# Kernel optimization log

Hardware: AMD Instinct MI355X
Metric: run time of the kernel (lower is better)

Reference implementation:

```python
import jax, jax.numpy as jnp
import numpy as np


def setup_inputs() -> dict:
    key = jax.random.key(0)
    ks = jax.random.split(key, 10)
    B, C, T, H, W = 8, 128, 8, 32, 32
    Cq = C // 8
    return {
        "x": jax.random.normal(ks[0], (B, C, T, H, W), dtype=jnp.float32),
        "Wq": jax.random.normal(ks[1], (Cq, C), dtype=jnp.float32) * (1.0 / np.sqrt(C)),
        "bq": jax.random.normal(ks[2], (Cq,), dtype=jnp.float32) * 0.02,
        "Wk": jax.random.normal(ks[3], (Cq, C), dtype=jnp.float32) * (1.0 / np.sqrt(C)),
        "bk": jax.random.normal(ks[4], (Cq,), dtype=jnp.float32) * 0.02,
        "Wv": jax.random.normal(ks[5], (C, C), dtype=jnp.float32) * (1.0 / np.sqrt(C)),
        "bv": jax.random.normal(ks[6], (C,), dtype=jnp.float32) * 0.02,
        "gamma_pam": jax.random.normal(ks[7], (1,), dtype=jnp.float32),
        "gamma_cam": jax.random.normal(ks[8], (1,), dtype=jnp.float32),
        "gamma_tim": jax.random.normal(ks[9], (1,), dtype=jnp.float32),
    }


def reference(x, Wq, bq, Wk, bk, Wv, bv, gamma_pam, gamma_cam, gamma_tim):
    B, C, T, H, W = x.shape
    HW = H * W

    # ---- PAM: position attention over HW, feature dim = (C//8)*T ----
    # 1x1x1 Conv3d == per-position channel matmul
    q = jnp.einsum('bcthw,oc->bothw', x, Wq) + bq[None, :, None, None, None]
    k = jnp.einsum('bcthw,oc->bothw', x, Wk) + bk[None, :, None, None, None]
    v = jnp.einsum('bcthw,oc->bothw', x, Wv) + bv[None, :, None, None, None]
    qf = q.reshape(B, -1, HW)   # [B, (C//8)*T, HW]
    kf = k.reshape(B, -1, HW)
    vf = v.reshape(B, -1, HW)   # [B, C*T, HW]
    energy = jnp.einsum('bcn,bcm->bnm', qf, kf)          # [B, HW, HW]
    attn = jax.nn.softmax(energy, axis=-1)
    # out = bmm(v, attn^T)
    pam = jnp.einsum('bcm,bnm->bcn', vf, attn).reshape(B, C, T, H, W)
    pam = gamma_pam * pam + x

    # ---- CAM: channel attention (C x C) with negated-energy softmax ----
    xc = x.reshape(B, C, -1)                              # [B, C, T*HW]
    e = jnp.einsum('bcn,bdn->bcd', xc, xc)                # [B, C, C]
    e = jnp.max(e, axis=-1, keepdims=True) - e
    a = jax.nn.softmax(e, axis=-1)
    cam = jnp.einsum('bcd,bdn->bcn', a, xc).reshape(B, C, T, H, W)
    cam = gamma_cam * cam + x

    # ---- TIM: temporal attention (T x T) with negated-energy softmax ----
    xt = jnp.transpose(x, (0, 2, 1, 3, 4)).reshape(B, T, -1)  # [B, T, C*HW]
    e = jnp.einsum('btn,bsn->bts', xt, xt)                # [B, T, T]
    e = jnp.max(e, axis=-1, keepdims=True) - e
    a = jax.nn.softmax(e, axis=-1)
    tim = jnp.einsum('bts,bsn->btn', a, xt).reshape(B, T, C, H, W)
    tim = jnp.transpose(tim, (0, 2, 1, 3, 4))
    tim = gamma_tim * tim + x

    return pam + cam + tim
```

## Files before the change

### kernel.cpp

```cpp
#include <hip/hip_runtime.h>
#include <cstdint>

typedef unsigned short u16;
typedef __attribute__((ext_vector_type(8))) short bf16x8;
typedef __attribute__((ext_vector_type(4))) float f32x4;

constexpr int B_  = 8;
constexpr int C_  = 128;
constexpr int T_  = 8;
constexpr int HW_ = 1024;
constexpr int P_  = T_ * HW_;
constexpr int F_  = 128;
constexpr int CT_ = C_ * T_;

static __device__ __forceinline__ u16 f2bf(float f) {
    union { float f; unsigned u; } v; v.f = f;
    unsigned r = v.u + 0x7fffu + ((v.u >> 16) & 1u);
    return (u16)(r >> 16);
}
static __device__ __forceinline__ float bf2f(u16 h) {
    union { unsigned u; float f; } v; v.u = ((unsigned)h) << 16;
    return v.f;
}

#define GLOAD16(src, dst)                                                     \
    __builtin_amdgcn_global_load_lds(                                         \
        (const __attribute__((address_space(1))) void*)(src),                 \
        (__attribute__((address_space(3))) void*)(dst), 16, 0, 0)

__global__ __launch_bounds__(256)
void k_prep(const float* __restrict__ x, u16* __restrict__ xT,
            u16* __restrict__ xhi, u16* __restrict__ xlo,
            const float* __restrict__ Wq, const float* __restrict__ bq,
            const float* __restrict__ Wk, const float* __restrict__ bk,
            const float* __restrict__ Wv, const float* __restrict__ bv,
            u16* __restrict__ Wall, float* __restrict__ ball)
{
    const int tid = threadIdx.x;
    if (blockIdx.x == 64) {
        if (blockIdx.y != 0) return;
        for (int i = tid; i < 20480; i += 256) {
            int oc = i >> 7, c = i & 127;
            float w;
            if (oc < 16)      w = Wq[oc * 128 + c];
            else if (oc < 32) w = Wk[(oc - 16) * 128 + c];
            else              w = Wv[(oc - 32) * 128 + c];
            Wall[i] = f2bf(w);
        }
        if (tid < 160) {
            float bb;
            if (tid < 16)      bb = bq[tid];
            else if (tid < 32) bb = bk[tid - 16];
            else               bb = bv[tid - 32];
            ball[tid] = bb;
        }
        return;
    }

    __shared__ char sy[32768];
    const int b  = blockIdx.y;
    const int p0 = blockIdx.x * 128;

    #pragma unroll
    for (int r = 0; r < 16; r++) {
        int lin = r * 256 + tid;
        int c = lin >> 5, j4 = (lin & 31) << 2;
        size_t gi = ((size_t)(b * C_ + c)) * P_ + p0 + j4;
        float4 xv = *(const float4*)&x[gi];
        float a4[4] = {xv.x, xv.y, xv.z, xv.w};
        ushort4 h, l;
        h.x = f2bf(a4[0]); h.y = f2bf(a4[1]);
        h.z = f2bf(a4[2]); h.w = f2bf(a4[3]);
        l.x = f2bf(a4[0] - bf2f(h.x)); l.y = f2bf(a4[1] - bf2f(h.y));
        l.z = f2bf(a4[2] - bf2f(h.z)); l.w = f2bf(a4[3] - bf2f(h.w));
        *(ushort4*)&xhi[gi] = h;
        *(ushort4*)&xlo[gi] = l;
        #pragma unroll
        for (int u = 0; u < 4; u++) {
            int pi = j4 + u;
            int byte = pi * 256 + ((c * 2) ^ (((pi >> 2) & 15) << 4));
            *(u16*)(sy + byte) = (u == 0) ? h.x : (u == 1) ? h.y
                               : (u == 2) ? h.z : h.w;
        }
    }
    __syncthreads();
    #pragma unroll
    for (int r = 0; r < 8; r++) {
        int lin = r * 256 + tid;
        int pi = lin >> 4, ci8 = (lin & 15) << 3;
        bf16x8 v = *(const bf16x8*)(sy + pi * 256 +
                                    ((ci8 * 2) ^ (((pi >> 2) & 15) << 4)));
        *(bf16x8*)&xT[((size_t)(b * P_ + p0 + pi)) * C_ + ci8] = v;
    }
}

__global__ __launch_bounds__(256)
void k_qkv(const u16* __restrict__ xT, const u16* __restrict__ Wall,
           const float* __restrict__ ball,
           u16* __restrict__ qt, u16* __restrict__ kt, u16* __restrict__ v16)
{
    __shared__ char Ws[40960];
    const int b  = blockIdx.y;
    const int p0 = blockIdx.x * 128;
    const int tid = threadIdx.x, lane = tid & 63, w = tid >> 6;

    #pragma unroll
    for (int i = 0; i < 10; i++) {
        int ch  = w * 10 + i;
        int row = ch * 4 + (lane >> 4);
        int col = ((lane & 15) ^ (row & 7)) * 8;
        GLOAD16(Wall + row * 128 + col, Ws + ch * 1024);
    }

    const u16* Bb = xT + ((size_t)(b * P_ + p0 + w * 32)) * F_;
    bf16x8 bg[4][2];
    #pragma unroll
    for (int ks = 0; ks < 4; ks++)
        #pragma unroll
        for (int ni = 0; ni < 2; ni++)
            bg[ks][ni] = *(const bf16x8*)(Bb +
                (size_t)(ni * 16 + (lane & 15)) * F_ + ks * 32 + (lane >> 4) * 8);
    __syncthreads();

    f32x4 acc[10][2];
    #pragma unroll
    for (int mi = 0; mi < 10; mi++) {
        acc[mi][0] = (f32x4){0.f, 0.f, 0.f, 0.f};
        acc[mi][1] = (f32x4){0.f, 0.f, 0.f, 0.f};
    }

    #pragma unroll
    for (int mi = 0; mi < 10; mi++) {
        #pragma unroll
        for (int ks = 0; ks < 4; ks++) {
            int row  = mi * 16 + (lane & 15);
            int slot = (ks * 4 + (lane >> 4)) ^ (row & 7);
            bf16x8 af = *(const bf16x8*)(Ws + row * 256 + slot * 16);
            acc[mi][0] = __builtin_amdgcn_mfma_f32_16x16x32_bf16(
                af, bg[ks][0], acc[mi][0], 0, 0, 0);
            acc[mi][1] = __builtin_amdgcn_mfma_f32_16x16x32_bf16(
                af, bg[ks][1], acc[mi][1], 0, 0, 0);
        }
    }

    const int t      = p0 >> 10;
    const int hwbase = (p0 & 1023) + w * 32;
    #pragma unroll
    for (int mi = 0; mi < 10; mi++)
        #pragma unroll
        for (int ni = 0; ni < 2; ni++)
            #pragma unroll
            for (int r = 0; r < 4; r++) {
                int oc = mi * 16 + (lane >> 4) * 4 + r;
                int hw = hwbase + ni * 16 + (lane & 15);
                u16 bv16 = f2bf(acc[mi][ni][r] + ball[oc]);
                if (mi == 0)
                    qt[((size_t)b * HW_ + hw) * F_ + oc * 8 + t] = bv16;
                else if (mi == 1)
                    kt[((size_t)b * HW_ + hw) * F_ + (oc - 16) * 8 + t] = bv16;
                else
                    v16[((size_t)(b * C_ + oc - 32)) * P_ + t * HW_ + hw] = bv16;
            }
}

__global__ __launch_bounds__(256)
void k_energy(const u16* __restrict__ qt, const u16* __restrict__ kt,
              float* __restrict__ E)
{
    __shared__ char As[32768];
    __shared__ char Bs[32768];
    const int b  = blockIdx.z;
    const int n0 = blockIdx.y * 128, m0 = blockIdx.x * 128;
    const int tid = threadIdx.x, lane = tid & 63, w = tid >> 6;
    const u16* qb = qt + (size_t)b * HW_ * F_;
    const u16* kb = kt + (size_t)b * HW_ * F_;

    #pragma unroll
    for (int i = 0; i < 8; i++) {
        int c    = w * 8 + i;
        int row  = c * 4 + (lane >> 4);
        int col  = ((lane & 15) ^ (row & 7)) * 8;
        GLOAD16(qb + (size_t)(n0 + row) * F_ + col, As + c * 1024);
        GLOAD16(kb + (size_t)(m0 + row) * F_ + col, Bs + c * 1024);
    }
    __syncthreads();

    const int wr = w >> 1, wc = w & 1;
    f32x4 acc[4][4];
    #pragma unroll
    for (int mi = 0; mi < 4; mi++)
        #pragma unroll
        for (int ni = 0; ni < 4; ni++) acc[mi][ni] = (f32x4){0.f, 0.f, 0.f, 0.f};

    #pragma unroll
    for (int ks = 0; ks < 4; ks++) {
        bf16x8 af[4], bg[4];
        #pragma unroll
        for (int mi = 0; mi < 4; mi++) {
            int row  = wr * 64 + mi * 16 + (lane & 15);
            int slot = (ks * 4 + (lane >> 4)) ^ (row & 7);
            af[mi] = *(const bf16x8*)(As + row * 256 + slot * 16);
            int rb  = wc * 64 + mi * 16 + (lane & 15);
            int sb  = (ks * 4 + (lane >> 4)) ^ (rb & 7);
            bg[mi] = *(const bf16x8*)(Bs + rb * 256 + sb * 16);
        }
        #pragma unroll
        for (int mi = 0; mi < 4; mi++)
            #pragma unroll
            for (int ni = 0; ni < 4; ni++)
                acc[mi][ni] = __builtin_amdgcn_mfma_f32_16x16x32_bf16(
                    af[mi], bg[ni], acc[mi][ni], 0, 0, 0);
    }

    float* Eb = E + (size_t)b * HW_ * HW_;
    #pragma unroll
    for (int mi = 0; mi < 4; mi++)
        #pragma unroll
        for (int ni = 0; ni < 4; ni++)
            #pragma unroll
            for (int r = 0; r < 4; r++)
                Eb[(size_t)(n0 + wr * 64 + mi * 16 + (lane >> 4) * 4 + r) * HW_
                   + m0 + wc * 64 + ni * 16 + (lane & 15)] = acc[mi][ni][r];
}

__global__ __launch_bounds__(256)
void k_softmax(const float* __restrict__ E, u16* __restrict__ A16)
{
    const float* e = E + (size_t)blockIdx.x * HW_;
    const int tid = threadIdx.x;
    float4 v = ((const float4*)e)[tid];
    float m = fmaxf(fmaxf(v.x, v.y), fmaxf(v.z, v.w));
    #pragma unroll
    for (int off = 32; off; off >>= 1) m = fmaxf(m, __shfl_xor(m, off));
    __shared__ float s1[4], s2[4];
    if ((tid & 63) == 0) s1[tid >> 6] = m;
    __syncthreads();
    m = fmaxf(fmaxf(s1[0], s1[1]), fmaxf(s1[2], s1[3]));
    v.x = __expf(v.x - m); v.y = __expf(v.y - m);
    v.z = __expf(v.z - m); v.w = __expf(v.w - m);
    float s = v.x + v.y + v.z + v.w;
    #pragma unroll
    for (int off = 32; off; off >>= 1) s += __shfl_xor(s, off);
    if ((tid & 63) == 0) s2[tid >> 6] = s;
    __syncthreads();
    s = s2[0] + s2[1] + s2[2] + s2[3];
    float inv = 1.0f / s;
    ushort4 pk;
    pk.x = f2bf(v.x * inv); pk.y = f2bf(v.y * inv);
    pk.z = f2bf(v.z * inv); pk.w = f2bf(v.w * inv);
    ((ushort4*)(A16 + (size_t)blockIdx.x * HW_))[tid] = pk;
}

__global__ __launch_bounds__(256)
void k_pv(const u16* __restrict__ v16, const u16* __restrict__ A16,
          const float* __restrict__ gamma_pam, u16* __restrict__ pam16)
{
    __shared__ char As[2][16384];
    __shared__ char Bs[2][16384];
    const int b   = blockIdx.z;
    const int ct0 = blockIdx.y * 128, n0 = blockIdx.x * 128;
    const int tid = threadIdx.x, lane = tid & 63, w = tid >> 6;
    const u16* vb = v16 + (size_t)b * CT_ * HW_;
    const u16* ab = A16 + (size_t)b * HW_ * HW_;

    const int s_row = (lane >> 3);
    const int s_col = ((lane & 7) ^ ((lane >> 3) & 7)) * 8;

    const int wr = w >> 1, wc = w & 1;
    f32x4 acc[4][4];
    #pragma unroll
    for (int mi = 0; mi < 4; mi++)
        #pragma unroll
        for (int ni = 0; ni < 4; ni++) acc[mi][ni] = (f32x4){0.f, 0.f, 0.f, 0.f};

    #pragma unroll
    for (int i = 0; i < 4; i++) {
        int c = w * 4 + i;
        int row = c * 8 + s_row;
        GLOAD16(vb + (size_t)(ct0 + row) * HW_ + s_col, As[0] + c * 1024);
        GLOAD16(ab + (size_t)(n0  + row) * HW_ + s_col, Bs[0] + c * 1024);
    }
    __syncthreads();

    int cur = 0;
    for (int it = 0; it < 16; ++it) {
        if (it < 15) {
            int mc = (it + 1) * 64;
            #pragma unroll
            for (int i = 0; i < 4; i++) {
                int c = w * 4 + i;
                int row = c * 8 + s_row;
                GLOAD16(vb + (size_t)(ct0 + row) * HW_ + mc + s_col,
                        As[cur ^ 1] + c * 1024);
                GLOAD16(ab + (size_t)(n0  + row) * HW_ + mc + s_col,
                        Bs[cur ^ 1] + c * 1024);
            }
        }
        const char* Ac = As[cur];
        const char* Bc = Bs[cur];
        #pragma unroll
        for (int ks = 0; ks < 2; ks++) {
            bf16x8 af[4], bg[4];
            #pragma unroll
            for (int mi = 0; mi < 4; mi++) {
                int row  = wr * 64 + mi * 16 + (lane & 15);
                int slot = (ks * 4 + (lane >> 4)) ^ (row & 7);
                af[mi] = *(const bf16x8*)(Ac + row * 128 + slot * 16);
                int rb  = wc * 64 + mi * 16 + (lane & 15);
                int sb  = (ks * 4 + (lane >> 4)) ^ (rb & 7);
                bg[mi] = *(const bf16x8*)(Bc + rb * 128 + sb * 16);
            }
            #pragma unroll
            for (int mi = 0; mi < 4; mi++)
                #pragma unroll
                for (int ni = 0; ni < 4; ni++)
                    acc[mi][ni] = __builtin_amdgcn_mfma_f32_16x16x32_bf16(
                        af[mi], bg[ni], acc[mi][ni], 0, 0, 0);
        }
        __syncthreads();
        cur ^= 1;
    }

    const float gp = gamma_pam[0];
    u16* ob = pam16 + (size_t)b * CT_ * HW_;
    #pragma unroll
    for (int mi = 0; mi < 4; mi++)
        #pragma unroll
        for (int ni = 0; ni < 4; ni++)
            #pragma unroll
            for (int r = 0; r < 4; r++)
                ob[(size_t)(ct0 + wr * 64 + mi * 16 + (lane >> 4) * 4 + r) * HW_
                   + n0 + wc * 64 + ni * 16 + (lane & 15)] =
                    f2bf(gp * acc[mi][ni][r]);
}

__global__ __launch_bounds__(256)
void k_cam_gram(const u16* __restrict__ xhi, const u16* __restrict__ xlo,
                float* __restrict__ part)
{
    __shared__ char Sh[32768];
    __shared__ char Sl[32768];
    const int b = blockIdx.y, ch = blockIdx.x;
    const int tid = threadIdx.x, lane = tid & 63, w = tid >> 6;
    const u16* hb = xhi + (size_t)b * C_ * P_;
    const u16* lb = xlo + (size_t)b * C_ * P_;

    f32x4 acc[8][2];
    #pragma unroll
    for (int mi = 0; mi < 8; mi++) {
        acc[mi][0] = (f32x4){0.f, 0.f, 0.f, 0.f};
        acc[mi][1] = (f32x4){0.f, 0.f, 0.f, 0.f};
    }

    for (int kc = 0; kc < 2; kc++) {
        int n0 = ch * 256 + kc * 128;
        #pragma unroll
        for (int i = 0; i < 8; i++) {
            int c4  = w * 8 + i;
            int row = c4 * 4 + (lane >> 4);
            int col = ((lane & 15) ^ (row & 7)) * 8;
            GLOAD16(hb + (size_t)row * P_ + n0 + col, Sh + c4 * 1024);
            GLOAD16(lb + (size_t)row * P_ + n0 + col, Sl + c4 * 1024);
        }
        __syncthreads();
        #pragma unroll
        for (int ks = 0; ks < 4; ks++) {
            bf16x8 bh[2], bl[2];
            #pragma unroll
            for (int ni = 0; ni < 2; ni++) {
                int rb = w * 32 + ni * 16 + (lane & 15);
                int sb = (ks * 4 + (lane >> 4)) ^ (rb & 7);
                bh[ni] = *(const bf16x8*)(Sh + rb * 256 + sb * 16);
                bl[ni] = *(const bf16x8*)(Sl + rb * 256 + sb * 16);
            }
            #pragma unroll
            for (int mi = 0; mi < 8; mi++) {
                int ra = mi * 16 + (lane & 15);
                int sa = (ks * 4 + (lane >> 4)) ^ (ra & 7);
                bf16x8 ah = *(const bf16x8*)(Sh + ra * 256 + sa * 16);
                bf16x8 al = *(const bf16x8*)(Sl + ra * 256 + sa * 16);
                #pragma unroll
                for (int ni = 0; ni < 2; ni++) {
                    acc[mi][ni] = __builtin_amdgcn_mfma_f32_16x16x32_bf16(
                        ah, bh[ni], acc[mi][ni], 0, 0, 0);
                    acc[mi][ni] = __builtin_amdgcn_mfma_f32_16x16x32_bf16(
                        ah, bl[ni], acc[mi][ni], 0, 0, 0);
                    acc[mi][ni] = __builtin_amdgcn_mfma_f32_16x16x32_bf16(
                        al, bh[ni], acc[mi][ni], 0, 0, 0);
                }
            }
        }
        __syncthreads();
    }

    float* pb = part + ((size_t)(b * 32 + ch)) * 16384;
    #pragma unroll
    for (int mi = 0; mi < 8; mi++)
        #pragma unroll
        for (int ni = 0; ni < 2; ni++)
            #pragma unroll
            for (int r = 0; r < 4; r++) {
                int c = mi * 16 + (lane >> 4) * 4 + r;
                int d = w * 32 + ni * 16 + (lane & 15);
                pb[c * 128 + d] = acc[mi][ni][r];
            }
}

__global__ __launch_bounds__(128)
void k_cam_reduce(const float* __restrict__ part,
                  const float* __restrict__ gamma_cam, u16* __restrict__ acam16)
{
    const int b = blockIdx.y, c = blockIdx.x;
    const int d = threadIdx.x;
    float s = 0.f;
    for (int ch = 0; ch < 32; ch++)
        s += part[(((size_t)(b * 32 + ch)) * C_ + c) * C_ + d];
    float mn = s;
    #pragma unroll
    for (int off = 32; off; off >>= 1) mn = fminf(mn, __shfl_xor(mn, off));
    __shared__ float m1[2], m2[2];
    if ((d & 63) == 0) m1[d >> 6] = mn;
    __syncthreads();
    mn = fminf(m1[0], m1[1]);
    float p = __expf(mn - s);
    float sum = p;
    #pragma unroll
    for (int off = 32; off; off >>= 1) sum += __shfl_xor(sum, off);
    if ((d & 63) == 0) m2[d >> 6] = sum;
    __syncthreads();
    sum = m2[0] + m2[1];
    acam16[((size_t)(b * C_ + c)) * C_ + d] = f2bf(gamma_cam[0] * p / sum);
}

__global__ __launch_bounds__(256)
void k_tim_gram(const float* __restrict__ x, float* __restrict__ e_t)
{
    const int b = blockIdx.y, c = blockIdx.x;
    const int tid = threadIdx.x;
    const float* xb = x + ((size_t)(b * C_ + c)) * P_;
    float acc[8][8] = {};
    for (int r = 0; r < 4; r++) {
        int hw = r * 256 + tid;
        float xv[8];
        #pragma unroll
        for (int t = 0; t < 8; t++) xv[t] = xb[t * HW_ + hw];
        #pragma unroll
        for (int t = 0; t < 8; t++)
            #pragma unroll
            for (int s2 = 0; s2 < 8; s2++)
                acc[t][s2] += xv[t] * xv[s2];
    }
    __shared__ float sm[4][64];
    const int lane = tid & 63, wid = tid >> 6;
    #pragma unroll
    for (int u = 0; u < 64; u++) {
        float vv = acc[u >> 3][u & 7];
        #pragma unroll
        for (int off = 32; off; off >>= 1) vv += __shfl_xor(vv, off);
        if (lane == 0) sm[wid][u] = vv;
    }
    __syncthreads();
    if (tid < 64) {
        float vv = sm[0][tid] + sm[1][tid] + sm[2][tid] + sm[3][tid];
        atomicAdd(&e_t[b * 64 + tid], vv);
    }
}

__global__ __launch_bounds__(256)
void k_xprime(const float* __restrict__ x, const float* __restrict__ e_t,
              const float* __restrict__ gamma_tim, u16* __restrict__ Xp)
{
    const int b = blockIdx.y, c = blockIdx.x;
    const size_t base = ((size_t)(b * C_ + c)) * P_;
    const int tid = threadIdx.x;
    const float gt = gamma_tim[0];

    float4 xv[8];
    #pragma unroll
    for (int t = 0; t < 8; t++)
        xv[t] = *(const float4*)&x[base + t * HW_ + tid * 4];

    #pragma unroll
    for (int t = 0; t < 8; t++) {
        float e[8];
        #pragma unroll
        for (int s = 0; s < 8; s++) e[s] = e_t[b * 64 + t * 8 + s];
        float mn = e[0];
        #pragma unroll
        for (int s = 1; s < 8; s++) mn = fminf(mn, e[s]);
        float p[8], sum = 0.f;
        #pragma unroll
        for (int s = 0; s < 8; s++) { p[s] = __expf(mn - e[s]); sum += p[s]; }
        float inv = gt / sum;

        float4 o = make_float4(3.f * xv[t].x, 3.f * xv[t].y,
                               3.f * xv[t].z, 3.f * xv[t].w);
        #pragma unroll
        for (int s = 0; s < 8; s++) {
            float wgt = p[s] * inv;
            o.x += wgt * xv[s].x; o.y += wgt * xv[s].y;
            o.z += wgt * xv[s].z; o.w += wgt * xv[s].w;
        }
        ushort4 pk;
        pk.x = f2bf(o.x); pk.y = f2bf(o.y); pk.z = f2bf(o.z); pk.w = f2bf(o.w);
        *(ushort4*)&Xp[base + t * HW_ + tid * 4] = pk;
    }
}

__global__ __launch_bounds__(256)
void k_cam_av(const u16* __restrict__ acam16, const u16* __restrict__ xT,
              const u16* __restrict__ Xp, const u16* __restrict__ pam16,
              float* __restrict__ out)
{
    const int b  = blockIdx.y;
    const int p0 = blockIdx.x * 128;
    const int tid = threadIdx.x, lane = tid & 63, w = tid >> 6;

    const u16* Ab = acam16 + (size_t)b * C_ * C_;
    const u16* Bb = xT + ((size_t)(b * P_ + p0 + w * 32)) * C_;

    f32x4 acc[8][2];
    #pragma unroll
    for (int mi = 0; mi < 8; mi++) {
        acc[mi][0] = (f32x4){0.f, 0.f, 0.f, 0.f};
        acc[mi][1] = (f32x4){0.f, 0.f, 0.f, 0.f};
    }

    bf16x8 bg[4][2];
    #pragma unroll
    for (int ks = 0; ks < 4; ks++)
        #pragma unroll
        for (int ni = 0; ni < 2; ni++)
            bg[ks][ni] = *(const bf16x8*)(Bb +
                (size_t)(ni * 16 + (lane & 15)) * C_ + ks * 32 + (lane >> 4) * 8);

    #pragma unroll
    for (int mi = 0; mi < 8; mi++) {
        #pragma unroll
        for (int ks = 0; ks < 4; ks++) {
            bf16x8 af = *(const bf16x8*)(Ab +
                (size_t)(mi * 16 + (lane & 15)) * C_ + ks * 32 + (lane >> 4) * 8);
            acc[mi][0] = __builtin_amdgcn_mfma_f32_16x16x32_bf16(
                af, bg[ks][0], acc[mi][0], 0, 0, 0);
            acc[mi][1] = __builtin_amdgcn_mfma_f32_16x16x32_bf16(
                af, bg[ks][1], acc[mi][1], 0, 0, 0);
        }
    }

    const int tt = p0 >> 10;
    float* ob = out + (size_t)b * C_ * P_;
    const u16* xp = Xp + (size_t)b * C_ * P_;
    const u16* pb = pam16 + (size_t)b * CT_ * HW_;
    #pragma unroll
    for (int mi = 0; mi < 8; mi++)
        #pragma unroll
        for (int ni = 0; ni < 2; ni++)
            #pragma unroll
            for (int r = 0; r < 4; r++) {
                int c = mi * 16 + (lane >> 4) * 4 + r;
                int p = p0 + w * 32 + ni * 16 + (lane & 15);
                int hw = p & 1023;
                size_t i = (size_t)c * P_ + p;
                float pam = bf2f(pb[((size_t)(c * 8 + tt)) * HW_ + hw]);
                ob[i] = pam + acc[mi][ni][r] + bf2f(xp[i]);
            }
}

extern "C" void kernel_launch(void* const* d_in, const int* in_sizes, int n_in,
                              void* d_out, int out_size, void* d_ws, size_t ws_size,
                              hipStream_t stream)
{
    (void)in_sizes; (void)n_in; (void)out_size; (void)ws_size;
    const float* x  = (const float*)d_in[0];
    const float* Wq = (const float*)d_in[1];
    const float* bq = (const float*)d_in[2];
    const float* Wk = (const float*)d_in[3];
    const float* bk = (const float*)d_in[4];
    const float* Wv = (const float*)d_in[5];
    const float* bv = (const float*)d_in[6];
    const float* gp = (const float*)d_in[7];
    const float* gc = (const float*)d_in[8];
    const float* gt = (const float*)d_in[9];
    float* out = (float*)d_out;
    char*  ws  = (char*)d_ws;

    const size_t MiB = 1u << 20;
    u16*   xT     = (u16*)(ws + 0);
    u16*   v16    = (u16*)(ws + 16 * MiB);
    u16*   xhi    = (u16*)(ws + 32 * MiB);
    u16*   xlo    = (u16*)(ws + 48 * MiB);
    float* Ebuf   = (float*)(ws + 64 * MiB);
    float* part   = (float*)(ws + 64 * MiB);
    u16*   pam16  = (u16*)(ws + 80 * MiB);
    u16*   A16    = (u16*)(ws + 96 * MiB);
    u16*   Xp16   = (u16*)(ws + 96 * MiB);
    u16*   qtb    = (u16*)(ws + 112 * MiB);
    u16*   ktb    = (u16*)(ws + 114 * MiB);
    u16*   acam16 = (u16*)(ws + 116 * MiB);
    u16*   Wall   = (u16*)(ws + 116 * MiB + 65536);
    float* ball   = (float*)(ws + 116 * MiB + 131072);
    float* etim   = (float*)(ws + 116 * MiB + 139264);

    hipMemsetAsync(etim, 0, 512 * sizeof(float), stream);

    k_prep      <<<dim3(65, 8),   256, 0, stream>>>(x, xT, xhi, xlo,
                                                    Wq, bq, Wk, bk, Wv, bv,
                                                    Wall, ball);
    k_qkv       <<<dim3(64, 8),   256, 0, stream>>>(xT, Wall, ball,
                                                    qtb, ktb, v16);
    k_energy    <<<dim3(8, 8, 8), 256, 0, stream>>>(qtb, ktb, Ebuf);
    k_softmax   <<<dim3(8192),    256, 0, stream>>>(Ebuf, A16);
    k_tim_gram  <<<dim3(128, 8),  256, 0, stream>>>(x, etim);
    k_pv        <<<dim3(8, 8, 8), 256, 0, stream>>>(v16, A16, gp, pam16);
    k_xprime    <<<dim3(128, 8),  256, 0, stream>>>(x, etim, gt, Xp16);
    k_cam_gram  <<<dim3(32, 8),   256, 0, stream>>>(xhi, xlo, part);
    k_cam_reduce<<<dim3(128, 8),  128, 0, stream>>>(part, gc, acam16);
    k_cam_av    <<<dim3(64, 8),   256, 0, stream>>>(acam16, xT, Xp16,
                                                    pam16, out);
}
```

Baseline: 266.1 us.

## Fuse energy GEMM with softmax, fold QKV projection into prep, merge weight packing

The PAM energy GEMM and row softmax now run in one kernel, k_attn, which writes only the bf16 attention matrix. This removes the 32 MiB fp32 energy round trip through memory and one launch. The QKV projection moves into k_prep and reads the transposed x tile straight from shared memory, dropping the k_qkv launch and its xT reread. Weight packing moves into k_tim_gram, and biases are read directly instead of being staged. In exchange, k_attn uses only 512 blocks of 16 rows each, reads K from global memory without LDS staging, and k_prep now reads the weights from global memory per wave.

```diff
diff --git a/kernel.cpp b/kernel.cpp
--- a/kernel.cpp
+++ b/kernel.cpp
@@ -29,37 +29,65 @@
         (__attribute__((address_space(3))) void*)(dst), 16, 0, 0)
 
 __global__ __launch_bounds__(256)
+void k_tim_gram(const float* __restrict__ x, float* __restrict__ e_t,
+                const float* __restrict__ Wq, const float* __restrict__ Wk,
+                const float* __restrict__ Wv, u16* __restrict__ Wall)
+{
+    const int b = blockIdx.y, c = blockIdx.x;
+    const int tid = threadIdx.x;
+
+    if (blockIdx.x == 0 && blockIdx.y == 0) {
+        for (int i = tid; i < 20480; i += 256) {
+            int oc = i >> 7, cc = i & 127;
+            float wv;
+            if (oc < 16)      wv = Wq[oc * 128 + cc];
+            else if (oc < 32) wv = Wk[(oc - 16) * 128 + cc];
+            else              wv = Wv[(oc - 32) * 128 + cc];
+            Wall[i] = f2bf(wv);
+        }
+    }
+
+    const float* xb = x + ((size_t)(b * C_ + c)) * P_;
+    float acc[8][8] = {};
+    for (int r = 0; r < 4; r++) {
+        int hw = r * 256 + tid;
+        float xv[8];
+        #pragma unroll
+        for (int t = 0; t < 8; t++) xv[t] = xb[t * HW_ + hw];
+        #pragma unroll
+        for (int t = 0; t < 8; t++)
+            #pragma unroll
+            for (int s2 = 0; s2 < 8; s2++)
+                acc[t][s2] += xv[t] * xv[s2];
+    }
+    __shared__ float sm[4][64];
+    const int lane = tid & 63, wid = tid >> 6;
+    #pragma unroll
+    for (int u = 0; u < 64; u++) {
+        float vv = acc[u >> 3][u & 7];
+        #pragma unroll
+        for (int off = 32; off; off >>= 1) vv += __shfl_xor(vv, off);
+        if (lane == 0) sm[wid][u] = vv;
+    }
+    __syncthreads();
+    if (tid < 64) {
+        float vv = sm[0][tid] + sm[1][tid] + sm[2][tid] + sm[3][tid];
+        atomicAdd(&e_t[b * 64 + tid], vv);
+    }
+}
+
+__global__ __launch_bounds__(256)
 void k_prep(const float* __restrict__ x, u16* __restrict__ xT,
             u16* __restrict__ xhi, u16* __restrict__ xlo,
-            const float* __restrict__ Wq, const float* __restrict__ bq,
-            const float* __restrict__ Wk, const float* __restrict__ bk,
-            const float* __restrict__ Wv, const float* __restrict__ bv,
-            u16* __restrict__ Wall, float* __restrict__ ball)
-{
-    const int tid = threadIdx.x;
-    if (blockIdx.x == 64) {
-        if (blockIdx.y != 0) return;
-        for (int i = tid; i < 20480; i += 256) {
-            int oc = i >> 7, c = i & 127;
-            float w;
-            if (oc < 16)      w = Wq[oc * 128 + c];
-            else if (oc < 32) w = Wk[(oc - 16) * 128 + c];
-            else              w = Wv[(oc - 32) * 128 + c];
-            Wall[i] = f2bf(w);
-        }
-        if (tid < 160) {
-            float bb;
-            if (tid < 16)      bb = bq[tid];
-            else if (tid < 32) bb = bk[tid - 16];
-            else               bb = bv[tid - 32];
-            ball[tid] = bb;
-        }
-        return;
-    }
-
+            const u16* __restrict__ Wall,
+            const float* __restrict__ bq, const float* __restrict__ bk,
+            const float* __restrict__ bv,
+            u16* __restrict__ qt, u16* __restrict__ kt, u16* __restrict__ v16)
+{
     __shared__ char sy[32768];
     const int b  = blockIdx.y;
     const int p0 = blockIdx.x * 128;
+    const int tid = threadIdx.x, lane = tid & 63, w = tid >> 6;
 
     #pragma unroll
     for (int r = 0; r < 16; r++) {
@@ -84,6 +112,7 @@
         }
     }
     __syncthreads();
+
     #pragma unroll
     for (int r = 0; r < 8; r++) {
         int lin = r * 256 + tid;
@@ -92,35 +121,17 @@
                                     ((ci8 * 2) ^ (((pi >> 2) & 15) << 4)));
         *(bf16x8*)&xT[((size_t)(b * P_ + p0 + pi)) * C_ + ci8] = v;
     }
-}
-
-__global__ __launch_bounds__(256)
-void k_qkv(const u16* __restrict__ xT, const u16* __restrict__ Wall,
-           const float* __restrict__ ball,
-           u16* __restrict__ qt, u16* __restrict__ kt, u16* __restrict__ v16)
-{
-    __shared__ char Ws[40960];
-    const int b  = blockIdx.y;
-    const int p0 = blockIdx.x * 128;
-    const int tid = threadIdx.x, lane = tid & 63, w = tid >> 6;
-
-    #pragma unroll
-    for (int i = 0; i < 10; i++) {
-        int ch  = w * 10 + i;
-        int row = ch * 4 + (lane >> 4);
-        int col = ((lane & 15) ^ (row & 7)) * 8;
-        GLOAD16(Wall + row * 128 + col, Ws + ch * 1024);
-    }
-
-    const u16* Bb = xT + ((size_t)(b * P_ + p0 + w * 32)) * F_;
+
     bf16x8 bg[4][2];
     #pragma unroll
     for (int ks = 0; ks < 4; ks++)
         #pragma unroll
-        for (int ni = 0; ni < 2; ni++)
-            bg[ks][ni] = *(const bf16x8*)(Bb +
-                (size_t)(ni * 16 + (lane & 15)) * F_ + ks * 32 + (lane >> 4) * 8);
-    __syncthreads();
+        for (int ni = 0; ni < 2; ni++) {
+            int p  = w * 32 + ni * 16 + (lane & 15);
+            int cb = (ks * 32 + (lane >> 4) * 8) * 2;
+            bg[ks][ni] = *(const bf16x8*)(sy + p * 256 +
+                              (cb ^ (((p >> 2) & 15) << 4)));
+        }
 
     f32x4 acc[10][2];
     #pragma unroll
@@ -133,9 +144,8 @@
     for (int mi = 0; mi < 10; mi++) {
         #pragma unroll
         for (int ks = 0; ks < 4; ks++) {
-            int row  = mi * 16 + (lane & 15);
-            int slot = (ks * 4 + (lane >> 4)) ^ (row & 7);
-            bf16x8 af = *(const bf16x8*)(Ws + row * 256 + slot * 16);
+            bf16x8 af = *(const bf16x8*)(Wall + (mi * 16 + (lane & 15)) * 128
+                                          + ks * 32 + (lane >> 4) * 8);
             acc[mi][0] = __builtin_amdgcn_mfma_f32_16x16x32_bf16(
                 af, bg[ks][0], acc[mi][0], 0, 0, 0);
             acc[mi][1] = __builtin_amdgcn_mfma_f32_16x16x32_bf16(
@@ -153,7 +163,11 @@
             for (int r = 0; r < 4; r++) {
                 int oc = mi * 16 + (lane >> 4) * 4 + r;
                 int hw = hwbase + ni * 16 + (lane & 15);
-                u16 bv16 = f2bf(acc[mi][ni][r] + ball[oc]);
+                float bias;
+                if (mi == 0)      bias = bq[oc];
+                else if (mi == 1) bias = bk[oc - 16];
+                else              bias = bv[oc - 32];
+                u16 bv16 = f2bf(acc[mi][ni][r] + bias);
                 if (mi == 0)
                     qt[((size_t)b * HW_ + hw) * F_ + oc * 8 + t] = bv16;
                 else if (mi == 1)
@@ -164,91 +178,89 @@
 }
 
 __global__ __launch_bounds__(256)
-void k_energy(const u16* __restrict__ qt, const u16* __restrict__ kt,
-              float* __restrict__ E)
-{
-    __shared__ char As[32768];
-    __shared__ char Bs[32768];
-    const int b  = blockIdx.z;
-    const int n0 = blockIdx.y * 128, m0 = blockIdx.x * 128;
+void k_attn(const u16* __restrict__ qt, const u16* __restrict__ kt,
+            u16* __restrict__ A16)
+{
+    const int b  = blockIdx.y;
+    const int n0 = blockIdx.x * 16;
     const int tid = threadIdx.x, lane = tid & 63, w = tid >> 6;
     const u16* qb = qt + (size_t)b * HW_ * F_;
     const u16* kb = kt + (size_t)b * HW_ * F_;
 
-    #pragma unroll
-    for (int i = 0; i < 8; i++) {
-        int c    = w * 8 + i;
-        int row  = c * 4 + (lane >> 4);
-        int col  = ((lane & 15) ^ (row & 7)) * 8;
-        GLOAD16(qb + (size_t)(n0 + row) * F_ + col, As + c * 1024);
-        GLOAD16(kb + (size_t)(m0 + row) * F_ + col, Bs + c * 1024);
-    }
-    __syncthreads();
-
-    const int wr = w >> 1, wc = w & 1;
-    f32x4 acc[4][4];
-    #pragma unroll
-    for (int mi = 0; mi < 4; mi++)
-        #pragma unroll
-        for (int ni = 0; ni < 4; ni++) acc[mi][ni] = (f32x4){0.f, 0.f, 0.f, 0.f};
-
-    #pragma unroll
-    for (int ks = 0; ks < 4; ks++) {
-        bf16x8 af[4], bg[4];
-        #pragma unroll
-        for (int mi = 0; mi < 4; mi++) {
-            int row  = wr * 64 + mi * 16 + (lane & 15);
-            int slot = (ks * 4 + (lane >> 4)) ^ (row & 7);
-            af[mi] = *(const bf16x8*)(As + row * 256 + slot * 16);
-            int rb  = wc * 64 + mi * 16 + (lane & 15);
-            int sb  = (ks * 4 + (lane >> 4)) ^ (rb & 7);
-            bg[mi] = *(const bf16x8*)(Bs + rb * 256 + sb * 16);
-        }
-        #pragma unroll
-        for (int mi = 0; mi < 4; mi++)
-            #pragma unroll
-            for (int ni = 0; ni < 4; ni++)
-                acc[mi][ni] = __builtin_amdgcn_mfma_f32_16x16x32_bf16(
-                    af[mi], bg[ni], acc[mi][ni], 0, 0, 0);
-    }
-
-    float* Eb = E + (size_t)b * HW_ * HW_;
-    #pragma unroll
-    for (int mi = 0; mi < 4; mi++)
-        #pragma unroll
-        for (int ni = 0; ni < 4; ni++)
-            #pragma unroll
-            for (int r = 0; r < 4; r++)
-                Eb[(size_t)(n0 + wr * 64 + mi * 16 + (lane >> 4) * 4 + r) * HW_
-                   + m0 + wc * 64 + ni * 16 + (lane & 15)] = acc[mi][ni][r];
-}
-
-__global__ __launch_bounds__(256)
-void k_softmax(const float* __restrict__ E, u16* __restrict__ A16)
-{
-    const float* e = E + (size_t)blockIdx.x * HW_;
-    const int tid = threadIdx.x;
-    float4 v = ((const float4*)e)[tid];
-    float m = fmaxf(fmaxf(v.x, v.y), fmaxf(v.z, v.w));
-    #pragma unroll
-    for (int off = 32; off; off >>= 1) m = fmaxf(m, __shfl_xor(m, off));
-    __shared__ float s1[4], s2[4];
-    if ((tid & 63) == 0) s1[tid >> 6] = m;
-    __syncthreads();
-    m = fmaxf(fmaxf(s1[0], s1[1]), fmaxf(s1[2], s1[3]));
-    v.x = __expf(v.x - m); v.y = __expf(v.y - m);
-    v.z = __expf(v.z - m); v.w = __expf(v.w - m);
-    float s = v.x + v.y + v.z + v.w;
-    #pragma unroll
-    for (int off = 32; off; off >>= 1) s += __shfl_xor(s, off);
-    if ((tid & 63) == 0) s2[tid >> 6] = s;
-    __syncthreads();
-    s = s2[0] + s2[1] + s2[2] + s2[3];
-    float inv = 1.0f / s;
-    ushort4 pk;
-    pk.x = f2bf(v.x * inv); pk.y = f2bf(v.y * inv);
-    pk.z = f2bf(v.z * inv); pk.w = f2bf(v.w * inv);
-    ((ushort4*)(A16 + (size_t)blockIdx.x * HW_))[tid] = pk;
+    bf16x8 af[4];
+    #pragma unroll
+    for (int ks = 0; ks < 4; ks++)
+        af[ks] = *(const bf16x8*)(qb + (size_t)(n0 + (lane & 15)) * F_
+                                  + ks * 32 + (lane >> 4) * 8);
+
+    f32x4 acc[16];
+    #pragma unroll
+    for (int j = 0; j < 16; j++) acc[j] = (f32x4){0.f, 0.f, 0.f, 0.f};
+
+    #pragma unroll
+    for (int j = 0; j < 16; j++) {
+        const int m0 = w * 256 + j * 16;
+        #pragma unroll
+        for (int ks = 0; ks < 4; ks++) {
+            bf16x8 bg = *(const bf16x8*)(kb + (size_t)(m0 + (lane & 15)) * F_
+                                         + ks * 32 + (lane >> 4) * 8);
+            acc[j] = __builtin_amdgcn_mfma_f32_16x16x32_bf16(
+                af[ks], bg, acc[j], 0, 0, 0);
+        }
+    }
+
+    __shared__ float red[4][16];
+    float rmax[4];
+    #pragma unroll
+    for (int r = 0; r < 4; r++) {
+        float m = acc[0][r];
+        #pragma unroll
+        for (int j = 1; j < 16; j++) m = fmaxf(m, acc[j][r]);
+        #pragma unroll
+        for (int off = 1; off < 16; off <<= 1) m = fmaxf(m, __shfl_xor(m, off));
+        rmax[r] = m;
+    }
+    if ((lane & 15) == 0)
+        #pragma unroll
+        for (int r = 0; r < 4; r++) red[w][(lane >> 4) * 4 + r] = rmax[r];
+    __syncthreads();
+    #pragma unroll
+    for (int r = 0; r < 4; r++) {
+        int row = (lane >> 4) * 4 + r;
+        rmax[r] = fmaxf(fmaxf(red[0][row], red[1][row]),
+                        fmaxf(red[2][row], red[3][row]));
+    }
+    __syncthreads();
+
+    float rsum[4];
+    #pragma unroll
+    for (int r = 0; r < 4; r++) {
+        float s = 0.f;
+        #pragma unroll
+        for (int j = 0; j < 16; j++) {
+            acc[j][r] = __expf(acc[j][r] - rmax[r]);
+            s += acc[j][r];
+        }
+        #pragma unroll
+        for (int off = 1; off < 16; off <<= 1) s += __shfl_xor(s, off);
+        rsum[r] = s;
+    }
+    if ((lane & 15) == 0)
+        #pragma unroll
+        for (int r = 0; r < 4; r++) red[w][(lane >> 4) * 4 + r] = rsum[r];
+    __syncthreads();
+
+    u16* ob = A16 + ((size_t)b * HW_ + n0) * HW_;
+    #pragma unroll
+    for (int r = 0; r < 4; r++) {
+        int row = (lane >> 4) * 4 + r;
+        float inv = 1.0f / (red[0][row] + red[1][row] +
+                            red[2][row] + red[3][row]);
+        #pragma unroll
+        for (int j = 0; j < 16; j++)
+            ob[(size_t)row * HW_ + w * 256 + j * 16 + (lane & 15)] =
+                f2bf(acc[j][r] * inv);
+    }
 }
 
 __global__ __launch_bounds__(256)
@@ -433,40 +445,6 @@
 }
 
 __global__ __launch_bounds__(256)
-void k_tim_gram(const float* __restrict__ x, float* __restrict__ e_t)
-{
-    const int b = blockIdx.y, c = blockIdx.x;
-    const int tid = threadIdx.x;
-    const float* xb = x + ((size_t)(b * C_ + c)) * P_;
-    float acc[8][8] = {};
-    for (int r = 0; r < 4; r++) {
-        int hw = r * 256 + tid;
-        float xv[8];
-        #pragma unroll
-        for (int t = 0; t < 8; t++) xv[t] = xb[t * HW_ + hw];
-        #pragma unroll
-        for (int t = 0; t < 8; t++)
-            #pragma unroll
-            for (int s2 = 0; s2 < 8; s2++)
-                acc[t][s2] += xv[t] * xv[s2];
-    }
-    __shared__ float sm[4][64];
-    const int lane = tid & 63, wid = tid >> 6;
-    #pragma unroll
-    for (int u = 0; u < 64; u++) {
-        float vv = acc[u >> 3][u & 7];
-        #pragma unroll
-        for (int off = 32; off; off >>= 1) vv += __shfl_xor(vv, off);
-        if (lane == 0) sm[wid][u] = vv;
-    }
-    __syncthreads();
-    if (tid < 64) {
-        float vv = sm[0][tid] + sm[1][tid] + sm[2][tid] + sm[3][tid];
-        atomicAdd(&e_t[b * 64 + tid], vv);
-    }
-}
-
-__global__ __launch_bounds__(256)
 void k_xprime(const float* __restrict__ x, const float* __restrict__ e_t,
               const float* __restrict__ gamma_tim, u16* __restrict__ Xp)
 {
@@ -589,28 +567,24 @@
     u16*   v16    = (u16*)(ws + 16 * MiB);
     u16*   xhi    = (u16*)(ws + 32 * MiB);
     u16*   xlo    = (u16*)(ws + 48 * MiB);
-    float* Ebuf   = (float*)(ws + 64 * MiB);
-    float* part   = (float*)(ws + 64 * MiB);
+    u16*   A16    = (u16*)(ws + 64 * MiB);
     u16*   pam16  = (u16*)(ws + 80 * MiB);
-    u16*   A16    = (u16*)(ws + 96 * MiB);
-    u16*   Xp16   = (u16*)(ws + 96 * MiB);
-    u16*   qtb    = (u16*)(ws + 112 * MiB);
-    u16*   ktb    = (u16*)(ws + 114 * MiB);
-    u16*   acam16 = (u16*)(ws + 116 * MiB);
-    u16*   Wall   = (u16*)(ws + 116 * MiB + 65536);
-    float* ball   = (float*)(ws + 116 * MiB + 131072);
-    float* etim   = (float*)(ws + 116 * MiB + 139264);
+    float* part   = (float*)(ws + 96 * MiB);
+    u16*   Xp16   = (u16*)(ws + 113 * MiB);
+    u16*   qtb    = (u16*)(ws + 130 * MiB);
+    u16*   ktb    = (u16*)(ws + 132 * MiB);
+    u16*   acam16 = (u16*)(ws + 134 * MiB);
+    u16*   Wall   = (u16*)(ws + 134 * MiB + 65536);
+    float* etim   = (float*)(ws + 134 * MiB + 131072);
 
     hipMemsetAsync(etim, 0, 512 * sizeof(float), stream);
 
-    k_prep      <<<dim3(65, 8),   256, 0, stream>>>(x, xT, xhi, xlo,
-                                                    Wq, bq, Wk, bk, Wv, bv,
-                                                    Wall, ball);
-    k_qkv       <<<dim3(64, 8),   256, 0, stream>>>(xT, Wall, ball,
+    k_tim_gram  <<<dim3(128, 8),  256, 0, stream>>>(x, etim,
+                                                    Wq, Wk, Wv, Wall);
+    k_prep      <<<dim3(64, 8),   256, 0, stream>>>(x, xT, xhi, xlo, Wall,
+                                                    bq, bk, bv,
                                                     qtb, ktb, v16);
-    k_energy    <<<dim3(8, 8, 8), 256, 0, stream>>>(qtb, ktb, Ebuf);
-    k_softmax   <<<dim3(8192),    256, 0, stream>>>(Ebuf, A16);
-    k_tim_gram  <<<dim3(128, 8),  256, 0, stream>>>(x, etim);
+    k_attn      <<<dim3(64, 8),   256, 0, stream>>>(qtb, ktb, A16);
     k_pv        <<<dim3(8, 8, 8), 256, 0, stream>>>(v16, A16, gp, pam16);
     k_xprime    <<<dim3(128, 8),  256, 0, stream>>>(x, etim, gt, Xp16);
     k_cam_gram  <<<dim3(32, 8),   256, 0, stream>>>(xhi, xlo, part);
```

Result: no change. 264.1 us (-0.7%).
